# Performance work log

Hardware: AMD Instinct MI355X
Metric: run time of the kernel (lower is better)

## Reference

```python
import jax, jax.numpy as jnp
import numpy as np

B, S, D = 2, 2048, 2048
H = 1024          # per-expert swiglu hidden
E = 16            # num_experts
K = 2             # top_k
T = B * S
CAP = (K * T) // E  # capacity = top_k * tokens / experts * capacity_factor(1.0) = 512


def setup_inputs() -> dict:
    key = jax.random.key(0)
    ks = jax.random.split(key, 10)
    s = 0.02
    return {
        "hidden_states": jax.random.normal(ks[0], (B, S, D), jnp.float32),
        "gate_w": jax.random.normal(ks[1], (D, E), jnp.float32) * s,
        "w1": jax.random.normal(ks[2], (E, D, H), jnp.float32) * s,
        "w3": jax.random.normal(ks[3], (E, D, H), jnp.float32) * s,
        "w2": jax.random.normal(ks[4], (E, H, D), jnp.float32) * s,
        "sw1": jax.random.normal(ks[5], (D, H), jnp.float32) * s,
        "sw3": jax.random.normal(ks[6], (D, H), jnp.float32) * s,
        "sw2": jax.random.normal(ks[7], (H, D), jnp.float32) * s,
        "coef_w": jax.random.normal(ks[8], (D, 2), jnp.float32) * s,
        "coef_b": jnp.zeros((2,), jnp.float32),
    }


def _topk_gating(logits):
    """GShard-style top-k capacity gating. logits: [T,E] (gate runs in fp32).
    Returns combine [T,E,C], dispatch [T,E,C], l_aux scalar, exp_counts [E]."""
    probs = jax.nn.softmax(logits, axis=-1)                     # [T,E]
    top_vals, top_idx = jax.lax.top_k(probs, K)                 # [T,K]
    gates = top_vals / jnp.sum(top_vals, -1, keepdims=True)     # renormalize top-k
    masks = jax.nn.one_hot(top_idx, E, dtype=probs.dtype)       # [T,K,E]

    prior = jnp.zeros((E,), probs.dtype)
    combine = jnp.zeros((T, E, CAP), probs.dtype)
    for kk in range(K):  # fixed tiny K, structurally distinct slots
        m = masks[:, kk]                                        # [T,E]
        loc = jnp.cumsum(m, axis=0) - m + prior                 # position in expert buffer
        prior = prior + jnp.sum(m, axis=0)
        keep = m * (loc < CAP)                                  # capacity drop
        pos = jnp.sum(loc * m, axis=1).astype(jnp.int32)        # [T]
        loc_oh = jax.nn.one_hot(pos, CAP, dtype=probs.dtype)    # [T,C]
        combine = combine + gates[:, kk, None, None] * keep[:, :, None] * loc_oh[:, None, :]
    dispatch = (combine > 0).astype(probs.dtype)

    # load-balancing aux loss over top-1 assignment (GShard/DeepSpeed convention)
    me = jnp.mean(probs, axis=0)                                # [E]
    ce = jnp.mean(masks[:, 0], axis=0)                          # [E]
    l_aux = jnp.sum(me * ce) * E
    exp_counts = jnp.sum(masks, axis=(0, 1)).astype(jnp.int32)  # tokens routed per expert
    return combine, dispatch, l_aux, exp_counts


def _swiglu(x, a, b, c):
    return (jax.nn.silu(x @ a) * (x @ b)) @ c


def reference(hidden_states, gate_w, w1, w3, w2, sw1, sw3, sw2, coef_w, coef_b):
    x = hidden_states.reshape(T, D)
    logits = (x.astype(jnp.float32) @ gate_w)                   # gate kept in fp32
    combine, dispatch, l_aux, exp_counts = _topk_gating(logits)

    # dispatch -> grouped expert swiglu -> combine
    xe = jnp.einsum('tec,td->ecd', dispatch.astype(x.dtype), x)         # [E,C,D]
    h = jax.nn.silu(jnp.einsum('ecd,edh->ech', xe, w1)) * jnp.einsum('ecd,edh->ech', xe, w3)
    ye = jnp.einsum('ech,ehd->ecd', h, w2)                              # [E,C,D]
    moe_out = jnp.einsum('tec,ecd->td', combine.astype(x.dtype), ye)    # [T,D]

    # shared-expert residual MLP + softmax coefficient combine
    mlp_out = _swiglu(x, sw1, sw3, sw2)                                 # [T,D]
    coef = jax.nn.softmax(x @ coef_w + coef_b, axis=-1)                 # [T,2]
    out = moe_out * coef[:, 0:1] + mlp_out * coef[:, 1:2]
    return out.reshape(B, S, D), l_aux, exp_counts
```

## Files before the change

kernel.cpp:

```cpp
#include <hip/hip_runtime.h>
#include <hip/hip_bf16.h>
#include <stdint.h>

#define T_TOK 4096
#define DIM   2048
#define HID   1024
#define NE    16
#define CAPE  512

typedef __bf16 bf16x8 __attribute__((ext_vector_type(8)));
typedef float  f32x4  __attribute__((ext_vector_type(4)));

__device__ __forceinline__ ushort f2bf(float f) {
    union { float f; uint32_t u; } v; v.f = f;
    uint32_t r = (v.u + 0x7FFFu + ((v.u >> 16) & 1u)) >> 16;
    return (ushort)r;
}
__device__ __forceinline__ float bf2f(ushort u) {
    union { uint32_t u; float f; } v; v.u = (uint32_t)u << 16; return v.f;
}
__device__ __forceinline__ void gload16(const void* g, void* lds) {
    __builtin_amdgcn_global_load_lds(
        (const __attribute__((address_space(1))) uint32_t*)g,
        (__attribute__((address_space(3))) uint32_t*)lds, 16, 0, 0);
}
#define VMCNT(n) asm volatile("s_waitcnt vmcnt(" #n ")" ::: "memory")

__global__ __launch_bounds__(256) void logits_kernel(
    const float* __restrict__ x, const float* __restrict__ gate_w,
    const float* __restrict__ coef_w, const float* __restrict__ coef_b,
    ushort* __restrict__ xb,
    int* __restrict__ topidx, float* __restrict__ gatesw,
    float* __restrict__ coefo, float* __restrict__ probs_part,
    float* __restrict__ laux)
{
    __shared__ float gws[18 * 512];
    __shared__ float wred[4][NE];
    int tid = threadIdx.x;
    int wv = tid >> 6, lane = tid & 63;
    int tbase = blockIdx.x * 16 + wv * 4;
    float acc[4][18];
#pragma unroll
    for (int tk = 0; tk < 4; ++tk)
#pragma unroll
        for (int o = 0; o < 18; ++o) acc[tk][o] = 0.f;

    for (int c = 0; c < 4; ++c) {
        int d0 = c * 512;
        __syncthreads();
        const float4* g4 = (const float4*)(gate_w + (size_t)d0 * NE);
        for (int i = tid; i < 2048; i += 256) {
            float4 v = g4[i];
            int dd = i >> 2, o0 = (i & 3) * 4;
            gws[(o0 + 0) * 512 + dd] = v.x;
            gws[(o0 + 1) * 512 + dd] = v.y;
            gws[(o0 + 2) * 512 + dd] = v.z;
            gws[(o0 + 3) * 512 + dd] = v.w;
        }
        for (int i = tid; i < 1024; i += 256) {
            float v = coef_w[(size_t)d0 * 2 + i];
            gws[(16 + (i & 1)) * 512 + (i >> 1)] = v;
        }
        __syncthreads();
#pragma unroll
        for (int tk = 0; tk < 4; ++tk) {
            int t = tbase + tk;
            const float* xr = x + (size_t)t * DIM + d0;
            float xv[8];
#pragma unroll
            for (int j = 0; j < 8; ++j) xv[j] = xr[j * 64 + lane];
#pragma unroll
            for (int j = 0; j < 8; ++j)
                xb[(size_t)t * DIM + d0 + j * 64 + lane] = f2bf(xv[j]);
#pragma unroll
            for (int o = 0; o < 18; ++o) {
                const float* gr = &gws[o * 512 + lane];
                float a = acc[tk][o];
#pragma unroll
                for (int j = 0; j < 8; ++j) a += xv[j] * gr[j * 64];
                acc[tk][o] = a;
            }
        }
    }
#pragma unroll
    for (int tk = 0; tk < 4; ++tk)
#pragma unroll
        for (int off = 32; off > 0; off >>= 1)
#pragma unroll
            for (int o = 0; o < 18; ++o)
                acc[tk][o] += __shfl_down(acc[tk][o], off, 64);

    if (lane == 0) {
        float ps[NE];
#pragma unroll
        for (int e = 0; e < NE; ++e) ps[e] = 0.f;
#pragma unroll
        for (int tk = 0; tk < 4; ++tk) {
            int t = tbase + tk;
            float lg[18];
#pragma unroll
            for (int o = 0; o < 18; ++o) lg[o] = acc[tk][o];
            float m = lg[0];
#pragma unroll
            for (int e = 1; e < NE; ++e) m = fmaxf(m, lg[e]);
            float p[NE];
            float ssum = 0.f;
#pragma unroll
            for (int e = 0; e < NE; ++e) { p[e] = expf(lg[e] - m); ssum += p[e]; }
            float inv = 1.f / ssum;
#pragma unroll
            for (int e = 0; e < NE; ++e) p[e] *= inv;
            int i1 = 0;
#pragma unroll
            for (int e = 1; e < NE; ++e) if (p[e] > p[i1]) i1 = e;
            int i2 = -1;
#pragma unroll
            for (int e = 0; e < NE; ++e) { if (e == i1) continue; if (i2 < 0 || p[e] > p[i2]) i2 = e; }
            float g0 = p[i1], g1 = p[i2], gs = g0 + g1;
            topidx[t * 2 + 0] = i1; topidx[t * 2 + 1] = i2;
            gatesw[t * 2 + 0] = g0 / gs; gatesw[t * 2 + 1] = g1 / gs;
            float c0 = lg[16] + coef_b[0], c1 = lg[17] + coef_b[1];
            float cm = fmaxf(c0, c1);
            float e0 = expf(c0 - cm), e1 = expf(c1 - cm);
            float cs = e0 + e1;
            coefo[t * 2 + 0] = e0 / cs; coefo[t * 2 + 1] = e1 / cs;
#pragma unroll
            for (int e = 0; e < NE; ++e) ps[e] += p[e];
        }
#pragma unroll
        for (int e = 0; e < NE; ++e) wred[wv][e] = ps[e];
    }
    __syncthreads();
    if (tid < NE)
        probs_part[blockIdx.x * NE + tid] =
            wred[0][tid] + wred[1][tid] + wred[2][tid] + wred[3][tid];
    if (blockIdx.x == 0 && tid == 0) laux[0] = 0.f;
}

__global__ __launch_bounds__(256) void scan_transpose(
    const int* __restrict__ topidx, const float* __restrict__ gatesw,
    const float* __restrict__ probs_part,
    int* __restrict__ sidx, float* __restrict__ swt,
    int* __restrict__ assign_token, int* __restrict__ nvalid,
    float* __restrict__ out_tail,
    const float* __restrict__ w1, const float* __restrict__ w3,
    const float* __restrict__ sw1, const float* __restrict__ sw3,
    const float* __restrict__ sw2,
    ushort* __restrict__ w1T, ushort* __restrict__ w3T,
    ushort* __restrict__ sw1T, ushort* __restrict__ sw3T, ushort* __restrict__ sw2T)
{
    __shared__ __align__(16) ushort tile[128][264];
    int tid = threadIdx.x;

    if (blockIdx.x < NE) {
        __shared__ int wcnt[4];
        __shared__ float fred[4];
        __shared__ int runs;
        __shared__ int cnt0s;
        int e = blockIdx.x;
        int wv = tid >> 6, ln = tid & 63;
        unsigned long long ltmask = (1ull << ln) - 1ull;
        if (tid == 0) runs = 0;
        __syncthreads();
        for (int kk = 0; kk < 2; ++kk) {
            for (int c = 0; c < T_TOK; c += 256) {
                int t = c + tid;
                bool m = (topidx[t * 2 + kk] == e);
                unsigned long long b = __ballot(m);
                int within = __popcll(b & ltmask);
                if (ln == 0) wcnt[wv] = __popcll(b);
                __syncthreads();
                int cross = 0;
                for (int w = 0; w < wv; ++w) cross += wcnt[w];
                int pos = runs + cross + within;
                if (m) {
                    bool keep = pos < CAPE;
                    sidx[t * 2 + kk] = keep ? (e * CAPE + pos) : -1;
                    swt[t * 2 + kk] = keep ? gatesw[t * 2 + kk] : 0.f;
                    if (keep) assign_token[e * CAPE + pos] = t;
                }
                __syncthreads();
                if (tid == 0) runs += wcnt[0] + wcnt[1] + wcnt[2] + wcnt[3];
                __syncthreads();
            }
            if (kk == 0 && tid == 0) cnt0s = runs;
            __syncthreads();
        }
        for (int p = runs + tid; p < CAPE; p += 256)
            assign_token[e * CAPE + p] = 0;
        float val = probs_part[tid * NE + e];
#pragma unroll
        for (int off = 32; off > 0; off >>= 1) val += __shfl_down(val, off, 64);
        if (ln == 0) fred[wv] = val;
        __syncthreads();
        if (tid == 0) {
            float psum = fred[0] + fred[1] + fred[2] + fred[3];
            int total = runs;
            nvalid[e] = min(CAPE, total);
            out_tail[1 + e] = (float)total;
            float term = (psum / (float)T_TOK) * ((float)cnt0s / (float)T_TOK) * (float)NE;
            atomicAdd(&out_tail[0], term);
        }
        return;
    }

    int id = blockIdx.x - NE;
    const float* in; ushort* outp; int R, C, tx, ty;
    if (id < 2048) {
        int seg = id >> 10;
        int rem = id & 1023;
        int e = rem >> 6;
        int r2 = rem & 63;
        R = DIM; C = HID; tx = r2 & 7; ty = r2 >> 3;
        in   = (seg ? w3 : w1) + (size_t)e * DIM * HID;
        outp = (seg ? w3T : w1T) + (size_t)e * HID * DIM;
    } else {
        int id2 = id - 2048;
        int seg = id2 >> 6;
        int r2 = id2 & 63;
        if (seg < 2) {
            R = DIM; C = HID; tx = r2 & 7; ty = r2 >> 3;
            in = seg ? sw3 : sw1; outp = seg ? sw3T : sw1T;
        } else {
            R = HID; C = DIM; tx = r2 & 3; ty = r2 >> 2;
            in = sw2; outp = sw2T;
        }
    }
    int r0 = tx * 256, c0 = ty * 128;
    int t31 = tid & 31, t8 = tid >> 5;

#pragma unroll
    for (int it = 0; it < 8; ++it) {
        int r4 = (it * 8 + t8) * 4;
        int c4 = t31 * 4;
        const float* ip = in + (size_t)(r0 + r4) * C + c0 + c4;
        float va[4][4];
        *(float4*)va[0] = *(const float4*)(ip);
        *(float4*)va[1] = *(const float4*)(ip + C);
        *(float4*)va[2] = *(const float4*)(ip + 2 * (size_t)C);
        *(float4*)va[3] = *(const float4*)(ip + 3 * (size_t)C);
#pragma unroll
        for (int j = 0; j < 4; ++j) {
            uint2 u;
            u.x = (uint32_t)f2bf(va[0][j]) | ((uint32_t)f2bf(va[1][j]) << 16);
            u.y = (uint32_t)f2bf(va[2][j]) | ((uint32_t)f2bf(va[3][j]) << 16);
            *(uint2*)&tile[c4 + j][r4] = u;
        }
    }
    __syncthreads();

#pragma unroll
    for (int it = 0; it < 16; ++it) {
        int c = it * 8 + t8;
        int k = t31 * 8;
        uint4 o = *(const uint4*)&tile[c][k];
        *(uint4*)(outp + (size_t)(c0 + c) * R + r0 + k) = o;
    }
}

__device__ __forceinline__ void stage_half_off(
    const ushort* __restrict__ G, int k0, char* region, int tid,
    size_t off0, size_t off1)
{
#pragma unroll
    for (int q = 0; q < 2; ++q) {
        int c = q * 512 + tid;
        int row = c >> 3;
        int cb = (c & 7) << 4;
        int scb = cb ^ ((row & 7) << 4);
        const ushort* src = G + (q ? off1 : off0) + k0 + (scb >> 1);
        gload16(src, region + ((c - (tid & 63)) << 4));
    }
}

__device__ __forceinline__ bf16x8 ldfrag(const char* lds, int region, int row, int cb) {
    return *(const bf16x8*)(lds + region + row * 128 + (cb ^ ((row & 7) << 4)));
}

template<int NB>
__device__ __forceinline__ void core_single(
    const ushort* __restrict__ A, const ushort* __restrict__ B,
    size_t a0, size_t a1, size_t a2, size_t a3,
    size_t b0, size_t b1, size_t b2, size_t b3,
    int K, char* lds, f32x4 (&acc)[8][NB], int tid)
{
    const int DB = 32768 + NB * 8192;
    int lane = tid & 63;
    int wid = tid >> 6;
    int wrow = wid >> 2, wcol = wid & 3;
    int l15 = lane & 15, hi = lane >> 4;

#pragma unroll
    for (int m = 0; m < 8; ++m)
#pragma unroll
        for (int n = 0; n < NB; ++n)
            acc[m][n] = (f32x4){0.f, 0.f, 0.f, 0.f};

    int nj = K >> 7;

    stage_half_off(A, 0, lds + 0,           tid, a0, a1);
    stage_half_off(A, 0, lds + 16384,       tid, a2, a3);
    stage_half_off(B, 0, lds + 32768,       tid, b0, b1);
    if (NB == 4) stage_half_off(B, 0, lds + 32768 + 16384, tid, b2, b3);
    stage_half_off(B, 64, lds + DB + 32768, tid, b0, b1);
    if (NB == 4) stage_half_off(B, 64, lds + DB + 32768 + 16384, tid, b2, b3);
    if (NB == 4) VMCNT(4); else VMCNT(2);
    __builtin_amdgcn_s_barrier();
    __builtin_amdgcn_sched_barrier(0);

    for (int j = 0; j < nj; ++j) {
        int k1 = (2 * j + 1) << 6, k2 = (2 * j + 2) << 6, k3 = (2 * j + 3) << 6;
        bool st = (j < nj - 1);
#pragma unroll
        for (int d = 0; d < 2; ++d) {
            char* LA = lds + d * DB;
            char* LB = LA + 32768;
            char* LAo = lds + (d ^ 1) * DB;
            bf16x8 bf[NB][2];
#pragma unroll
            for (int p = 0; p < 4; ++p) {
                if (p == 0) {
#pragma unroll
                    for (int n = 0; n < NB; ++n)
#pragma unroll
                        for (int ks = 0; ks < 2; ++ks)
                            bf[n][ks] = ldfrag(LB, 0, wcol * (16 * NB) + n * 16 + l15, ks * 64 + hi * 16);
                }
                bf16x8 af[2][2];
#pragma unroll
                for (int i = 0; i < 2; ++i)
#pragma unroll
                    for (int ks = 0; ks < 2; ++ks)
                        af[i][ks] = ldfrag(LA, 0, wrow * 128 + (2 * p + i) * 16 + l15, ks * 64 + hi * 16);
                if (d == 0) {
                    if (p == 0)      stage_half_off(A, k1, LAo,         tid, a0, a1);
                    else if (p == 1) stage_half_off(A, k1, LAo + 16384, tid, a2, a3);
                    else if (p == 2) { if (st) stage_half_off(B, k2, LB, tid, b0, b1); }
                    else             { if (st && NB == 4) stage_half_off(B, k2, LB + 16384, tid, b2, b3); }
                } else {
                    if (st) {
                        if (p == 0)      stage_half_off(A, k2, LAo,         tid, a0, a1);
                        else if (p == 1) stage_half_off(A, k2, LAo + 16384, tid, a2, a3);
                        else if (p == 2) stage_half_off(B, k3, LB, tid, b0, b1);
                        else             { if (NB == 4) stage_half_off(B, k3, LB + 16384, tid, b2, b3); }
                    }
                }
                __builtin_amdgcn_s_barrier();
                if (p == 3) {
                    if (d == 0) {
                        if (st) { if (NB == 4) VMCNT(4); else VMCNT(2); }
                        else    VMCNT(0);
                    } else if (st) {
                        if (NB == 4) VMCNT(4); else VMCNT(2);
                    }
                }
                asm volatile("s_waitcnt lgkmcnt(0)" ::: "memory");
                __builtin_amdgcn_sched_barrier(0);
                __builtin_amdgcn_s_setprio(1);
#pragma unroll
                for (int i = 0; i < 2; ++i)
#pragma unroll
                    for (int n = 0; n < NB; ++n)
#pragma unroll
                        for (int ks = 0; ks < 2; ++ks)
                            acc[2 * p + i][n] = __builtin_amdgcn_mfma_f32_16x16x32_bf16(
                                af[i][ks], bf[n][ks], acc[2 * p + i][n], 0, 0, 0);
                __builtin_amdgcn_s_setprio(0);
                __builtin_amdgcn_s_barrier();
                __builtin_amdgcn_sched_barrier(0);
            }
        }
    }
}

template<int NM>
__device__ __forceinline__ void core_dual(
    const ushort* __restrict__ A, const ushort* __restrict__ B1,
    const ushort* __restrict__ B3,
    size_t a0, size_t a1, size_t a2, size_t a3,
    size_t b0, size_t b1,
    int K, char* lds, f32x4 (&acc1)[8][NM], f32x4 (&acc3)[8][NM], int tid)
{
    const int DB = 32768 + NM * 16384;
    int lane = tid & 63;
    int wid = tid >> 6;
    int wrow = wid >> 2, wcol = wid & 3;
    int l15 = lane & 15, hi = lane >> 4;

#pragma unroll
    for (int m = 0; m < 8; ++m)
#pragma unroll
        for (int n = 0; n < NM; ++n) {
            acc1[m][n] = (f32x4){0.f, 0.f, 0.f, 0.f};
            acc3[m][n] = (f32x4){0.f, 0.f, 0.f, 0.f};
        }

    int nj = K >> 7;

    stage_half_off(A, 0, lds + 0,     tid, a0, a1);
    stage_half_off(A, 0, lds + 16384, tid, a2, a3);
    stage_half_off(B1, 0, lds + 32768, tid, b0, b1);
    if (NM == 2) stage_half_off(B3, 0, lds + 32768 + 16384, tid, b0, b1);
    stage_half_off(B1, 64, lds + DB + 32768, tid, b0, b1);
    if (NM == 2) stage_half_off(B3, 64, lds + DB + 32768 + 16384, tid, b0, b1);
    if (NM == 2) VMCNT(4); else VMCNT(2);
    __builtin_amdgcn_s_barrier();
    __builtin_amdgcn_sched_barrier(0);

    for (int j = 0; j < nj; ++j) {
        int k1 = (2 * j + 1) << 6, k2 = (2 * j + 2) << 6, k3 = (2 * j + 3) << 6;
        bool st = (j < nj - 1);
#pragma unroll
        for (int d = 0; d < 2; ++d) {
            char* LA = lds + d * DB;
            char* LB = LA + 32768;
            char* LAo = lds + (d ^ 1) * DB;
            bf16x8 bf1[NM][2], bf3[NM][2];
#pragma unroll
            for (int p = 0; p < 4; ++p) {
                if (p == 0) {
#pragma unroll
                    for (int n = 0; n < NM; ++n)
#pragma unroll
                        for (int ks = 0; ks < 2; ++ks) {
                            int brow = wcol * (16 * NM) + n * 16 + l15;
                            bf1[n][ks] = ldfrag(LB, 0, brow,           ks * 64 + hi * 16);
                            bf3[n][ks] = ldfrag(LB, 0, brow + NM * 64, ks * 64 + hi * 16);
                        }
                }
                bf16x8 af[2][2];
#pragma unroll
                for (int i = 0; i < 2; ++i)
#pragma unroll
                    for (int ks = 0; ks < 2; ++ks)
                        af[i][ks] = ldfrag(LA, 0, wrow * 128 + (2 * p + i) * 16 + l15, ks * 64 + hi * 16);
                if (d == 0) {
                    if (p == 0)      stage_half_off(A, k1, LAo,         tid, a0, a1);
                    else if (p == 1) stage_half_off(A, k1, LAo + 16384, tid, a2, a3);
                    else if (p == 2) { if (st) stage_half_off(B1, k2, LB, tid, b0, b1); }
                    else             { if (st && NM == 2) stage_half_off(B3, k2, LB + 16384, tid, b0, b1); }
                } else {
                    if (st) {
                        if (p == 0)      stage_half_off(A, k2, LAo,         tid, a0, a1);
                        else if (p == 1) stage_half_off(A, k2, LAo + 16384, tid, a2, a3);
                        else if (p == 2) stage_half_off(B1, k3, LB, tid, b0, b1);
                        else             { if (NM == 2) stage_half_off(B3, k3, LB + 16384, tid, b0, b1); }
                    }
                }
                __builtin_amdgcn_s_barrier();
                if (p == 3) {
                    if (d == 0) {
                        if (st) { if (NM == 2) VMCNT(4); else VMCNT(2); }
                        else    VMCNT(0);
                    } else if (st) {
                        if (NM == 2) VMCNT(4); else VMCNT(2);
                    }
                }
                asm volatile("s_waitcnt lgkmcnt(0)" ::: "memory");
                __builtin_amdgcn_sched_barrier(0);
                __builtin_amdgcn_s_setprio(1);
#pragma unroll
                for (int i = 0; i < 2; ++i)
#pragma unroll
                    for (int n = 0; n < NM; ++n)
#pragma unroll
                        for (int ks = 0; ks < 2; ++ks) {
                            acc1[2 * p + i][n] = __builtin_amdgcn_mfma_f32_16x16x32_bf16(
                                af[i][ks], bf1[n][ks], acc1[2 * p + i][n], 0, 0, 0);
                            acc3[2 * p + i][n] = __builtin_amdgcn_mfma_f32_16x16x32_bf16(
                                af[i][ks], bf3[n][ks], acc3[2 * p + i][n], 0, 0, 0);
                        }
                __builtin_amdgcn_s_setprio(0);
                __builtin_amdgcn_s_barrier();
                __builtin_amdgcn_sched_barrier(0);
            }
        }
    }
}

__global__ __launch_bounds__(512, 2) void gemm8_up(
    const ushort* __restrict__ xb,
    const ushort* __restrict__ w1T, const ushort* __restrict__ w3T,
    const ushort* __restrict__ sw1T, const ushort* __restrict__ sw3T,
    const int* __restrict__ assign_token,
    ushort* __restrict__ HH, const int* __restrict__ nvalid)
{
    __shared__ __align__(16) char lds[131072];
    int b = blockIdx.x;
    int tid = threadIdx.x;
    int rr = tid >> 3;
    int lane = tid & 63, wid = tid >> 6;
    int wrow = wid >> 2, wcol = wid & 3;

    if (b < 256) {
        int id = (b & 7) * 32 + (b >> 3);
        int e = id >> 4, rem = id & 15;
        int mt = rem >> 3, nt = rem & 7;
        int bm = mt * 256, bn = nt * 128;
        if (bm >= nvalid[e]) return;
        const int* at = assign_token + e * CAPE + bm;
        size_t a0 = (size_t)at[rr] * DIM;
        size_t a1 = (size_t)at[64 + rr] * DIM;
        size_t a2 = (size_t)at[128 + rr] * DIM;
        size_t a3 = (size_t)at[192 + rr] * DIM;
        const ushort* B1 = w1T + (size_t)e * HID * DIM;
        const ushort* B3 = w3T + (size_t)e * HID * DIM;
        size_t b0 = (size_t)(bn + rr) * DIM;
        size_t b1 = (size_t)(bn + 64 + rr) * DIM;
        f32x4 acc1[8][2], acc3[8][2];
        core_dual<2>(xb, B1, B3, a0, a1, a2, a3, b0, b1, DIM, lds, acc1, acc3, tid);
        ushort* O = HH + (size_t)e * CAPE * HID;
        int rbase = bm + wrow * 128 + (lane >> 4) * 4;
        int cbase = bn + wcol * 32 + (lane & 15);
#pragma unroll
        for (int m = 0; m < 8; ++m)
#pragma unroll
            for (int n = 0; n < 2; ++n) {
                int col = cbase + n * 16;
#pragma unroll
                for (int r = 0; r < 4; ++r) {
                    float g = acc1[m][n][r];
                    float s = g / (1.f + __expf(-g));
                    O[(size_t)(rbase + m * 16 + r) * HID + col] = f2bf(s * acc3[m][n][r]);
                }
            }
    } else {
        int b2 = b - 256;
        int id = (b2 & 7) * 32 + (b2 >> 3);
        int mt = id >> 4, nt = id & 15;
        int bm = mt * 256, bn = nt * 64;
        size_t a0 = (size_t)(bm + rr) * DIM;
        size_t a1 = (size_t)(bm + 64 + rr) * DIM;
        size_t a2 = (size_t)(bm + 128 + rr) * DIM;
        size_t a3 = (size_t)(bm + 192 + rr) * DIM;
        size_t b0 = (size_t)(bn + rr) * DIM;
        size_t b1 = (size_t)(sw3T - sw1T) + (size_t)(bn + rr) * DIM;
        f32x4 acc1[8][1], acc3[8][1];
        core_dual<1>(xb, sw1T, sw1T, a0, a1, a2, a3, b0, b1, DIM, lds, acc1, acc3, tid);
        ushort* O = HH + (size_t)NE * CAPE * HID;
        int rbase = bm + wrow * 128 + (lane >> 4) * 4;
        int col = bn + wcol * 16 + (lane & 15);
#pragma unroll
        for (int m = 0; m < 8; ++m)
#pragma unroll
            for (int r = 0; r < 4; ++r) {
                float g = acc1[m][0][r];
                float s = g / (1.f + __expf(-g));
                O[(size_t)(rbase + m * 16 + r) * HID + col] = f2bf(s * acc3[m][0][r]);
            }
    }
}

__global__ __launch_bounds__(512, 2) void gemm8_down(
    const ushort* __restrict__ HH, const float* __restrict__ w2f,
    const ushort* __restrict__ sw2T, ushort* __restrict__ ye,
    ushort* __restrict__ mlpb, const float* __restrict__ coefo,
    const int* __restrict__ nvalid)
{
    __shared__ __align__(16) char lds[131072];
    int b = blockIdx.x;
    int tid = threadIdx.x;
    int rr = tid >> 3;
    int lane = tid & 63, wid = tid >> 6;
    int wrow = wid >> 2, wcol = wid & 3;

    if (b < 256) {
        int id = (b & 7) * 32 + (b >> 3);
        int e = id >> 4, rem = id & 15;
        int mt = rem >> 3, nt = rem & 7;
        int bm = mt * 256, bn = nt * 256;
        if (bm >= nvalid[e]) return;
        const ushort* A = HH + (size_t)e * CAPE * HID;
        const float*  W = w2f + (size_t)e * HID * DIM;
        ushort* Ob = ye + (size_t)e * CAPE * DIM;
        size_t a0 = (size_t)(bm + rr) * HID;
        size_t a1 = (size_t)(bm + 64 + rr) * HID;
        size_t a2 = (size_t)(bm + 128 + rr) * HID;
        size_t a3 = (size_t)(bm + 192 + rr) * HID;
        int nq = tid & 63;
        int kb = (tid >> 6) * 8;
        int l15 = lane & 15, hi = lane >> 4;

        f32x4 acc[8][4];
#pragma unroll
        for (int m = 0; m < 8; ++m)
#pragma unroll
            for (int n = 0; n < 4; ++n)
                acc[m][n] = (f32x4){0.f, 0.f, 0.f, 0.f};

        float4 breg[8];
        stage_half_off(A, 0, lds + 0,     tid, a0, a1);
        stage_half_off(A, 0, lds + 16384, tid, a2, a3);
        {
            const float* src = W + (size_t)kb * DIM + bn + nq * 4;
#pragma unroll
            for (int kk = 0; kk < 8; ++kk)
                breg[kk] = *(const float4*)(src + (size_t)kk * DIM);
        }
        {
            char* LB = lds + 32768;
#pragma unroll
            for (int j = 0; j < 4; ++j) {
                int r = nq * 4 + j;
                ushort pk[8];
#pragma unroll
                for (int kk = 0; kk < 8; ++kk) pk[kk] = f2bf(((const float*)&breg[kk])[j]);
                int cb = (kb * 2) ^ ((r & 7) << 4);
                *(uint4*)(LB + r * 128 + cb) = *(uint4*)pk;
            }
        }
        VMCNT(0);
        __syncthreads();

        int d = 0;
        for (int t = 0; t < HID / 64; ++t) {
            bool pf = (t < HID / 64 - 1);
            char* LA = lds + d * 65536;
            char* LB = LA + 32768;
            char* LAo = lds + (d ^ 1) * 65536;
            char* LBo = LAo + 32768;
            if (pf) {
                int k0 = (t + 1) * 64;
                stage_half_off(A, k0, LAo,         tid, a0, a1);
                stage_half_off(A, k0, LAo + 16384, tid, a2, a3);
                const float* src = W + (size_t)(k0 + kb) * DIM + bn + nq * 4;
#pragma unroll
                for (int kk = 0; kk < 8; ++kk)
                    breg[kk] = *(const float4*)(src + (size_t)kk * DIM);
            }
#pragma unroll
            for (int ks = 0; ks < 2; ++ks) {
                bf16x8 af[8], bf[4];
#pragma unroll
                for (int m = 0; m < 8; ++m)
                    af[m] = ldfrag(LA, 0, wrow * 128 + m * 16 + l15, ks * 64 + hi * 16);
#pragma unroll
                for (int n = 0; n < 4; ++n)
                    bf[n] = ldfrag(LB, 0, wcol * 64 + n * 16 + l15, ks * 64 + hi * 16);
#pragma unroll
                for (int m = 0; m < 8; ++m)
#pragma unroll
                    for (int n = 0; n < 4; ++n)
                        acc[m][n] = __builtin_amdgcn_mfma_f32_16x16x32_bf16(
                            af[m], bf[n], acc[m][n], 0, 0, 0);
            }
            if (pf) {
#pragma unroll
                for (int j = 0; j < 4; ++j) {
                    int r = nq * 4 + j;
                    ushort pk[8];
#pragma unroll
                    for (int kk = 0; kk < 8; ++kk) pk[kk] = f2bf(((const float*)&breg[kk])[j]);
                    int cb = (kb * 2) ^ ((r & 7) << 4);
                    *(uint4*)(LBo + r * 128 + cb) = *(uint4*)pk;
                }
            }
            VMCNT(0);
            __syncthreads();
            d ^= 1;
        }

        int rbase = bm + wrow * 128 + (lane >> 4) * 4;
        int cbase = bn + wcol * 64 + (lane & 15);
#pragma unroll
        for (int m = 0; m < 8; ++m)
#pragma unroll
            for (int n = 0; n < 4; ++n) {
                int col = cbase + n * 16;
#pragma unroll
                for (int r = 0; r < 4; ++r)
                    Ob[(size_t)(rbase + m * 16 + r) * DIM + col] = f2bf(acc[m][n][r]);
            }
    } else {
        int b2i = b - 256;
        int id = (b2i & 7) * 32 + (b2i >> 3);
        int mt = id >> 4, nt = id & 15;
        int bm = mt * 256, bn = nt * 128;
        const ushort* A = HH + (size_t)NE * CAPE * HID;
        const ushort* B = sw2T;
        size_t a0 = (size_t)(bm + rr) * HID;
        size_t a1 = (size_t)(bm + 64 + rr) * HID;
        size_t a2 = (size_t)(bm + 128 + rr) * HID;
        size_t a3 = (size_t)(bm + 192 + rr) * HID;
        size_t b0 = (size_t)(bn + rr) * HID;
        size_t b1 = (size_t)(bn + 64 + rr) * HID;
        f32x4 acc[8][2];
        core_single<2>(A, B, a0, a1, a2, a3, b0, b1, 0, 0, HID, lds, acc, tid);
        int rbase = bm + wrow * 128 + (lane >> 4) * 4;
        int cbase = bn + wcol * 32 + (lane & 15);
#pragma unroll
        for (int m = 0; m < 8; ++m)
#pragma unroll
            for (int n = 0; n < 2; ++n) {
                int col = cbase + n * 16;
#pragma unroll
                for (int r = 0; r < 4; ++r) {
                    int row = rbase + m * 16 + r;
                    mlpb[(size_t)row * DIM + col] = f2bf(acc[m][n][r] * coefo[2 * row + 1]);
                }
            }
    }
}

__global__ __launch_bounds__(256) void combine_kernel(
    const ushort* __restrict__ ye, const ushort* __restrict__ mlpb,
    const int* __restrict__ sidx, const float* __restrict__ swt,
    const float* __restrict__ coefo, float* __restrict__ out)
{
    int idx = blockIdx.x * 256 + threadIdx.x;
    int t = idx >> 9;
    int d = (idx & 511) << 2;
    int s0 = sidx[t * 2], s1 = sidx[t * 2 + 1];
    float c0 = coefo[t * 2];
    float w0 = swt[t * 2] * c0, w1 = swt[t * 2 + 1] * c0;
    uint2 mb = *(const uint2*)(mlpb + (size_t)t * DIM + d);
    const ushort* mp = (const ushort*)&mb;
    float4 v;
    v.x = bf2f(mp[0]); v.y = bf2f(mp[1]); v.z = bf2f(mp[2]); v.w = bf2f(mp[3]);
    if (s0 >= 0) {
        uint2 y = *(const uint2*)(ye + (size_t)s0 * DIM + d);
        const ushort* yp = (const ushort*)&y;
        v.x += w0 * bf2f(yp[0]); v.y += w0 * bf2f(yp[1]);
        v.z += w0 * bf2f(yp[2]); v.w += w0 * bf2f(yp[3]);
    }
    if (s1 >= 0) {
        uint2 y = *(const uint2*)(ye + (size_t)s1 * DIM + d);
        const ushort* yp = (const ushort*)&y;
        v.x += w1 * bf2f(yp[0]); v.y += w1 * bf2f(yp[1]);
        v.z += w1 * bf2f(yp[2]); v.w += w1 * bf2f(yp[3]);
    }
    *(float4*)(out + (size_t)t * DIM + d) = v;
}

extern "C" void kernel_launch(void* const* d_in, const int* in_sizes, int n_in,
                              void* d_out, int out_size, void* d_ws, size_t ws_size,
                              hipStream_t stream)
{
    const float* x      = (const float*)d_in[0];
    const float* gate_w = (const float*)d_in[1];
    const float* w1     = (const float*)d_in[2];
    const float* w3     = (const float*)d_in[3];
    const float* w2     = (const float*)d_in[4];
    const float* sw1    = (const float*)d_in[5];
    const float* sw3    = (const float*)d_in[6];
    const float* sw2    = (const float*)d_in[7];
    const float* coef_w = (const float*)d_in[8];
    const float* coef_b = (const float*)d_in[9];
    float* out = (float*)d_out;

    char* ws = (char*)d_ws;
    size_t off = 0;
    auto alloc = [&](size_t bytes) -> void* {
        void* p = ws + off;
        off += (bytes + 255) & ~(size_t)255;
        return p;
    };
    int*    nvalid       = (int*)alloc(NE * 4);
    int*    topidx       = (int*)alloc((size_t)T_TOK * 2 * 4);
    float*  gatesw       = (float*)alloc((size_t)T_TOK * 2 * 4);
    float*  coefo        = (float*)alloc((size_t)T_TOK * 2 * 4);
    int*    sidx         = (int*)alloc((size_t)T_TOK * 2 * 4);
    float*  swt          = (float*)alloc((size_t)T_TOK * 2 * 4);
    int*    assign_token = (int*)alloc((size_t)NE * CAPE * 4);
    float*  probs_part   = (float*)alloc((size_t)256 * NE * 4);
    ushort* w1T  = (ushort*)alloc((size_t)NE * HID * DIM * 2);
    ushort* w3T  = (ushort*)alloc((size_t)NE * HID * DIM * 2);
    ushort* sw1T = (ushort*)alloc((size_t)HID * DIM * 2);
    ushort* sw3T = (ushort*)alloc((size_t)HID * DIM * 2);
    ushort* sw2T = (ushort*)alloc((size_t)DIM * HID * 2);
    ushort* xb   = (ushort*)alloc((size_t)T_TOK * DIM * 2);
    size_t HROWS = (size_t)NE * CAPE + T_TOK;
    ushort* HH   = (ushort*)alloc(HROWS * HID * 2);
    ushort* ye   = (ushort*)alloc((size_t)NE * CAPE * DIM * 2);
    ushort* mlpb = (ushort*)alloc((size_t)T_TOK * DIM * 2);

    float* out_tail = out + (size_t)T_TOK * DIM;

    logits_kernel<<<T_TOK / 16, 256, 0, stream>>>(
        x, gate_w, coef_w, coef_b, xb, topidx, gatesw, coefo, probs_part, out_tail);
    scan_transpose<<<NE + 2240, 256, 0, stream>>>(
        topidx, gatesw, probs_part, sidx, swt, assign_token, nvalid, out_tail,
        w1, w3, sw1, sw3, sw2, w1T, w3T, sw1T, sw3T, sw2T);
    gemm8_up<<<512, 512, 0, stream>>>(xb, w1T, w3T, sw1T, sw3T, assign_token, HH, nvalid);
    gemm8_down<<<512, 512, 0, stream>>>(HH, w2, sw2T, ye, mlpb, coefo, nvalid);
    combine_kernel<<<(T_TOK * (DIM / 4)) / 256, 256, 0, stream>>>(
        ye, mlpb, sidx, swt, coefo, out);
}
```

Measured before the change: 390.9 us.

## Split gating into per-token logits kernel and separate softmax/top-k finish kernel

```diff
diff --git a/kernel.cpp b/kernel.cpp
--- a/kernel.cpp
+++ b/kernel.cpp
@@ -28,113 +28,99 @@
 
 __global__ __launch_bounds__(256) void logits_kernel(
     const float* __restrict__ x, const float* __restrict__ gate_w,
-    const float* __restrict__ coef_w, const float* __restrict__ coef_b,
-    ushort* __restrict__ xb,
+    const float* __restrict__ coef_w, float* __restrict__ logits,
+    ushort* __restrict__ xb)
+{
+    int t = blockIdx.x * 4 + (threadIdx.x >> 6);
+    int lane = threadIdx.x & 63;
+    const float* xr = x + (size_t)t * DIM;
+    float acc[18];
+#pragma unroll
+    for (int o = 0; o < 18; ++o) acc[o] = 0.f;
+#pragma unroll
+    for (int g = 0; g < DIM / 512; ++g) {
+        int d = g * 512 + lane * 8;
+        float4 a = *(const float4*)(xr + d);
+        float4 b4 = *(const float4*)(xr + d + 4);
+        float xv[8] = {a.x, a.y, a.z, a.w, b4.x, b4.y, b4.z, b4.w};
+        ushort ob[8];
+#pragma unroll
+        for (int j = 0; j < 8; ++j) {
+            const float* gw = gate_w + (size_t)(d + j) * NE;
+#pragma unroll
+            for (int o = 0; o < NE; ++o) acc[o] += xv[j] * gw[o];
+            acc[16] += xv[j] * coef_w[(d + j) * 2 + 0];
+            acc[17] += xv[j] * coef_w[(d + j) * 2 + 1];
+            ob[j] = f2bf(xv[j]);
+        }
+        *(uint4*)(xb + (size_t)t * DIM + d) = *(uint4*)ob;
+    }
+#pragma unroll
+    for (int off = 32; off > 0; off >>= 1) {
+#pragma unroll
+        for (int o = 0; o < 18; ++o) acc[o] += __shfl_down(acc[o], off, 64);
+    }
+    if (lane == 0) {
+#pragma unroll
+        for (int o = 0; o < 18; ++o) logits[(size_t)t * 18 + o] = acc[o];
+    }
+}
+
+__global__ __launch_bounds__(256) void finish_kernel(
+    const float* __restrict__ logits, const float* __restrict__ coef_b,
     int* __restrict__ topidx, float* __restrict__ gatesw,
     float* __restrict__ coefo, float* __restrict__ probs_part,
     float* __restrict__ laux)
 {
-    __shared__ float gws[18 * 512];
     __shared__ float wred[4][NE];
-    int tid = threadIdx.x;
-    int wv = tid >> 6, lane = tid & 63;
-    int tbase = blockIdx.x * 16 + wv * 4;
-    float acc[4][18];
-#pragma unroll
-    for (int tk = 0; tk < 4; ++tk)
-#pragma unroll
-        for (int o = 0; o < 18; ++o) acc[tk][o] = 0.f;
-
-    for (int c = 0; c < 4; ++c) {
-        int d0 = c * 512;
-        __syncthreads();
-        const float4* g4 = (const float4*)(gate_w + (size_t)d0 * NE);
-        for (int i = tid; i < 2048; i += 256) {
-            float4 v = g4[i];
-            int dd = i >> 2, o0 = (i & 3) * 4;
-            gws[(o0 + 0) * 512 + dd] = v.x;
-            gws[(o0 + 1) * 512 + dd] = v.y;
-            gws[(o0 + 2) * 512 + dd] = v.z;
-            gws[(o0 + 3) * 512 + dd] = v.w;
-        }
-        for (int i = tid; i < 1024; i += 256) {
-            float v = coef_w[(size_t)d0 * 2 + i];
-            gws[(16 + (i & 1)) * 512 + (i >> 1)] = v;
-        }
-        __syncthreads();
-#pragma unroll
-        for (int tk = 0; tk < 4; ++tk) {
-            int t = tbase + tk;
-            const float* xr = x + (size_t)t * DIM + d0;
-            float xv[8];
-#pragma unroll
-            for (int j = 0; j < 8; ++j) xv[j] = xr[j * 64 + lane];
-#pragma unroll
-            for (int j = 0; j < 8; ++j)
-                xb[(size_t)t * DIM + d0 + j * 64 + lane] = f2bf(xv[j]);
-#pragma unroll
-            for (int o = 0; o < 18; ++o) {
-                const float* gr = &gws[o * 512 + lane];
-                float a = acc[tk][o];
-#pragma unroll
-                for (int j = 0; j < 8; ++j) a += xv[j] * gr[j * 64];
-                acc[tk][o] = a;
-            }
-        }
-    }
-#pragma unroll
-    for (int tk = 0; tk < 4; ++tk)
-#pragma unroll
-        for (int off = 32; off > 0; off >>= 1)
-#pragma unroll
-            for (int o = 0; o < 18; ++o)
-                acc[tk][o] += __shfl_down(acc[tk][o], off, 64);
-
-    if (lane == 0) {
-        float ps[NE];
-#pragma unroll
-        for (int e = 0; e < NE; ++e) ps[e] = 0.f;
-#pragma unroll
-        for (int tk = 0; tk < 4; ++tk) {
-            int t = tbase + tk;
-            float lg[18];
-#pragma unroll
-            for (int o = 0; o < 18; ++o) lg[o] = acc[tk][o];
-            float m = lg[0];
-#pragma unroll
-            for (int e = 1; e < NE; ++e) m = fmaxf(m, lg[e]);
-            float p[NE];
-            float ssum = 0.f;
-#pragma unroll
-            for (int e = 0; e < NE; ++e) { p[e] = expf(lg[e] - m); ssum += p[e]; }
-            float inv = 1.f / ssum;
-#pragma unroll
-            for (int e = 0; e < NE; ++e) p[e] *= inv;
-            int i1 = 0;
-#pragma unroll
-            for (int e = 1; e < NE; ++e) if (p[e] > p[i1]) i1 = e;
-            int i2 = -1;
-#pragma unroll
-            for (int e = 0; e < NE; ++e) { if (e == i1) continue; if (i2 < 0 || p[e] > p[i2]) i2 = e; }
-            float g0 = p[i1], g1 = p[i2], gs = g0 + g1;
-            topidx[t * 2 + 0] = i1; topidx[t * 2 + 1] = i2;
-            gatesw[t * 2 + 0] = g0 / gs; gatesw[t * 2 + 1] = g1 / gs;
-            float c0 = lg[16] + coef_b[0], c1 = lg[17] + coef_b[1];
-            float cm = fmaxf(c0, c1);
-            float e0 = expf(c0 - cm), e1 = expf(c1 - cm);
-            float cs = e0 + e1;
-            coefo[t * 2 + 0] = e0 / cs; coefo[t * 2 + 1] = e1 / cs;
-#pragma unroll
-            for (int e = 0; e < NE; ++e) ps[e] += p[e];
-        }
-#pragma unroll
-        for (int e = 0; e < NE; ++e) wred[wv][e] = ps[e];
+    int t = blockIdx.x * 256 + threadIdx.x;
+    float lg[18];
+#pragma unroll
+    for (int o = 0; o < 18; ++o) lg[o] = logits[(size_t)t * 18 + o];
+    float p[NE];
+    float m = lg[0];
+#pragma unroll
+    for (int e = 1; e < NE; ++e) m = fmaxf(m, lg[e]);
+    float ssum = 0.f;
+#pragma unroll
+    for (int e = 0; e < NE; ++e) { p[e] = expf(lg[e] - m); ssum += p[e]; }
+    float inv = 1.f / ssum;
+#pragma unroll
+    for (int e = 0; e < NE; ++e) p[e] *= inv;
+    int i1 = 0;
+#pragma unroll
+    for (int e = 1; e < NE; ++e) if (p[e] > p[i1]) i1 = e;
+    int i2 = -1;
+#pragma unroll
+    for (int e = 0; e < NE; ++e) { if (e == i1) continue; if (i2 < 0 || p[e] > p[i2]) i2 = e; }
+    float g0 = p[i1], g1 = p[i2], gs = g0 + g1;
+    topidx[t * 2 + 0] = i1; topidx[t * 2 + 1] = i2;
+    gatesw[t * 2 + 0] = g0 / gs; gatesw[t * 2 + 1] = g1 / gs;
+    float c0 = lg[16] + coef_b[0], c1 = lg[17] + coef_b[1];
+    float cm = fmaxf(c0, c1);
+    float e0 = expf(c0 - cm), e1 = expf(c1 - cm);
+    float cs = e0 + e1;
+    coefo[t * 2 + 0] = e0 / cs; coefo[t * 2 + 1] = e1 / cs;
+
+    float r[NE];
+#pragma unroll
+    for (int e = 0; e < NE; ++e) r[e] = p[e];
+#pragma unroll
+    for (int off = 32; off > 0; off >>= 1) {
+#pragma unroll
+        for (int e = 0; e < NE; ++e) r[e] += __shfl_down(r[e], off, 64);
+    }
+    int wv = threadIdx.x >> 6, ln = threadIdx.x & 63;
+    if (ln == 0) {
+#pragma unroll
+        for (int e = 0; e < NE; ++e) wred[wv][e] = r[e];
     }
     __syncthreads();
-    if (tid < NE)
-        probs_part[blockIdx.x * NE + tid] =
-            wred[0][tid] + wred[1][tid] + wred[2][tid] + wred[3][tid];
-    if (blockIdx.x == 0 && tid == 0) laux[0] = 0.f;
+    if (threadIdx.x < NE)
+        probs_part[blockIdx.x * NE + threadIdx.x] =
+            wred[0][threadIdx.x] + wred[1][threadIdx.x]
+          + wred[2][threadIdx.x] + wred[3][threadIdx.x];
+    if (blockIdx.x == 0 && threadIdx.x == 0) laux[0] = 0.f;
 }
 
 __global__ __launch_bounds__(256) void scan_transpose(
@@ -188,7 +174,7 @@
         }
         for (int p = runs + tid; p < CAPE; p += 256)
             assign_token[e * CAPE + p] = 0;
-        float val = probs_part[tid * NE + e];
+        float val = (tid < 16) ? probs_part[tid * NE + e] : 0.f;
 #pragma unroll
         for (int off = 32; off > 0; off >>= 1) val += __shfl_down(val, off, 64);
         if (ln == 0) fred[wv] = val;
@@ -762,7 +748,8 @@
     int*    sidx         = (int*)alloc((size_t)T_TOK * 2 * 4);
     float*  swt          = (float*)alloc((size_t)T_TOK * 2 * 4);
     int*    assign_token = (int*)alloc((size_t)NE * CAPE * 4);
-    float*  probs_part   = (float*)alloc((size_t)256 * NE * 4);
+    float*  probs_part   = (float*)alloc((size_t)16 * NE * 4);
+    float*  logits       = (float*)alloc((size_t)T_TOK * 18 * 4);
     ushort* w1T  = (ushort*)alloc((size_t)NE * HID * DIM * 2);
     ushort* w3T  = (ushort*)alloc((size_t)NE * HID * DIM * 2);
     ushort* sw1T = (ushort*)alloc((size_t)HID * DIM * 2);
@@ -776,8 +763,9 @@
 
     float* out_tail = out + (size_t)T_TOK * DIM;
 
-    logits_kernel<<<T_TOK / 16, 256, 0, stream>>>(
-        x, gate_w, coef_w, coef_b, xb, topidx, gatesw, coefo, probs_part, out_tail);
+    logits_kernel<<<T_TOK / 4, 256, 0, stream>>>(x, gate_w, coef_w, logits, xb);
+    finish_kernel<<<T_TOK / 256, 256, 0, stream>>>(logits, coef_b, topidx, gatesw,
+                                                   coefo, probs_part, out_tail);
     scan_transpose<<<NE + 2240, 256, 0, stream>>>(
         topidx, gatesw, probs_part, sidx, swt, assign_token, nvalid, out_tail,
         w1, w3, sw1, sw3, sw2, w1T, w3T, sw1T, sw3T, sw2T);
```

Result: faster. 355.9 us, median of 2 (-9.0%).
